# Kernel tuning notes

Measured on AMD Instinct MI355X. Metric: run time of the kernel, lower is better.

Reference implementation:

```python
import jax, jax.numpy as jnp
import numpy as np

N_NODES = 50000
N_EDGES = 1600000
NODE_DIM = 64
HIDDEN_DIM = 128
EDGE_DIM = 32


def _linear_params(key, fan_in, fan_out, bias=True):
    k1, k2 = jax.random.split(key)
    bound = 1.0 / np.sqrt(fan_in)
    W = jax.random.uniform(k1, (fan_in, fan_out), minval=-bound, maxval=bound, dtype=jnp.float32)
    if bias:
        b = jax.random.uniform(k2, (fan_out,), minval=-bound, maxval=bound, dtype=jnp.float32)
        return W, b
    return W, None


def setup_inputs() -> dict:
    key = jax.random.key(0)
    ks = jax.random.split(key, 12)
    h = jax.random.normal(ks[0], (N_NODES, NODE_DIM), dtype=jnp.float32)
    x = jax.random.normal(ks[1], (N_NODES, 3), dtype=jnp.float32) * 10.0
    edge_index = jax.random.randint(ks[2], (2, N_EDGES), 0, N_NODES, dtype=jnp.int32).astype(jnp.int64)
    edge_dist = jax.random.uniform(ks[3], (N_EDGES,), dtype=jnp.float32) * 10.0

    msg_in = 2 * NODE_DIM + EDGE_DIM
    node_w1, node_b1 = _linear_params(ks[4], msg_in, HIDDEN_DIM)
    node_w2, node_b2 = _linear_params(ks[5], HIDDEN_DIM, NODE_DIM)
    coord_w1, coord_b1 = _linear_params(ks[6], msg_in, HIDDEN_DIM)
    coord_w2, _ = _linear_params(ks[7], HIDDEN_DIM, 1, bias=False)
    edge_w1, edge_b1 = _linear_params(ks[8], 1, EDGE_DIM)
    edge_w2, edge_b2 = _linear_params(ks[9], EDGE_DIM, EDGE_DIM)

    return dict(h=h, x=x, edge_index=edge_index, edge_dist=edge_dist,
                node_w1=node_w1, node_b1=node_b1, node_w2=node_w2, node_b2=node_b2,
                coord_w1=coord_w1, coord_b1=coord_b1, coord_w2=coord_w2,
                edge_w1=edge_w1, edge_b1=edge_b1, edge_w2=edge_w2, edge_b2=edge_b2)


def reference(h, x, edge_index, edge_dist,
              node_w1, node_b1, node_w2, node_b2,
              coord_w1, coord_b1, coord_w2,
              edge_w1, edge_b1, edge_w2, edge_b2):
    src = edge_index[0]
    dst = edge_index[1]

    # edge_mlp: Linear(1, edge_dim) -> SiLU -> Linear(edge_dim, edge_dim)
    edge_attr = jax.nn.silu(edge_dist[:, None] @ edge_w1 + edge_b1) @ edge_w2 + edge_b2

    # per-edge message input: [E, 2*node_dim + edge_dim]
    m_input = jnp.concatenate([h[src], h[dst], edge_attr], axis=-1)

    # node_mlp: Linear -> SiLU -> Linear
    m = jax.nn.silu(m_input @ node_w1 + node_b1) @ node_w2 + node_b2
    h_agg = jnp.zeros_like(h).at[dst].add(m)

    # coord_mlp: Linear -> SiLU -> Linear(hidden, 1, bias=False)
    coord_weight = jax.nn.silu(m_input @ coord_w1 + coord_b1) @ coord_w2  # [E, 1]

    dir_vec = x[src] - x[dst]                               # [E, 3]
    dir_len = jnp.maximum(jnp.linalg.norm(dir_vec, axis=-1, keepdims=True), 1e-8)
    coord_update = coord_weight * (dir_vec / dir_len)
    x_agg = jnp.zeros_like(x).at[dst].add(coord_update)

    return (h + h_agg, x + x_agg)
```

## Files before the change

kernel.cpp:

```cpp
#include <hip/hip_runtime.h>
#include <stdint.h>

#define NN 50000
#define NE 1600000
#define BE 128

typedef __attribute__((ext_vector_type(8))) short short8;
typedef __attribute__((ext_vector_type(4))) float f32x4;

__device__ __forceinline__ unsigned short f2bf(float f) {
    unsigned int u = __float_as_uint(f);
    u += 0x7fff + ((u >> 16) & 1);
    return (unsigned short)(u >> 16);
}

__device__ __forceinline__ float silu_f(float v) {
    return v / (1.0f + __expf(-v));
}

__global__ void prep_kernel(const float* __restrict__ nw1,
                            const float* __restrict__ cw1,
                            const float* __restrict__ nw2,
                            unsigned short* __restrict__ ws) {
    int i = blockIdx.x * 256 + threadIdx.x;
    if (i < 20480) {
        int n = i / 160, k = i % 160;
        ws[i] = f2bf(nw1[k * 128 + n]);
    } else if (i < 40960) {
        int j = i - 20480; int n = j / 160, k = j % 160;
        ws[i] = f2bf(cw1[k * 128 + n]);
    } else if (i < 49152) {
        int j = i - 40960; int o = j / 128, k = j % 128;
        ws[i] = f2bf(nw2[k * 64 + o]);
    }
}

__global__ void init_out(const float4* __restrict__ h4,
                         const float4* __restrict__ x4,
                         float4* __restrict__ out4) {
    int i = blockIdx.x * 256 + threadIdx.x;
    if (i < 800000)       out4[i] = h4[i];
    else if (i < 837500)  out4[i] = x4[i - 800000];
}

#define MIS 168

__global__ __launch_bounds__(256, 3)
void egnn_edge_kernel(const float* __restrict__ h,
                      const float* __restrict__ x,
                      const int* __restrict__ eidx,
                      const float* __restrict__ edist,
                      const float* __restrict__ node_b1,
                      const float* __restrict__ node_b2,
                      const float* __restrict__ coord_b1,
                      const float* __restrict__ coord_w2,
                      const float* __restrict__ ew1,
                      const float* __restrict__ eb1,
                      const float* __restrict__ ew2,
                      const float* __restrict__ eb2,
                      const unsigned short* __restrict__ ws,
                      float* __restrict__ out_h,
                      float* __restrict__ out_x) {
    __shared__ unsigned short mi[BE * MIS];

    const int tid  = threadIdx.x;
    const int w    = tid >> 6;
    const int lane = tid & 63;
    const int ln   = lane & 15;
    const int quad = lane >> 4;
    const int e0   = blockIdx.x * BE;

    {
        const float4* h4 = (const float4*)h;
        const int g = tid >> 4, l16 = tid & 15;
        #pragma unroll
        for (int it = 0; it < 16; ++it) {
            int row = it * 16 + g;
            int e = row & 127;
            int node = (row < 128) ? eidx[e0 + e] : eidx[NE + e0 + e];
            int cbase = (row < 128) ? 0 : 64;
            float4 v = h4[node * 16 + l16];
            unsigned short b[4] = {f2bf(v.x), f2bf(v.y), f2bf(v.z), f2bf(v.w)};
            *(uint2*)&mi[e * MIS + cbase + l16 * 4] = *(uint2*)b;
        }
    }
    {
        int e = tid >> 1, half = tid & 1;
        float d = edist[e0 + e];
        float s[16];
        #pragma unroll
        for (int jj = 0; jj < 16; ++jj) s[jj] = eb2[half * 16 + jj];
        #pragma unroll
        for (int k = 0; k < 32; ++k) {
            float tk = silu_f(d * ew1[k] + eb1[k]);
            const float* r2 = ew2 + k * 32 + half * 16;
            #pragma unroll
            for (int jj = 0; jj < 16; ++jj) s[jj] += tk * r2[jj];
        }
        unsigned short sb[16];
        #pragma unroll
        for (int jj = 0; jj < 16; ++jj) sb[jj] = f2bf(s[jj]);
        *(uint4*)&mi[e * MIS + 128 + half * 16]     = *(uint4*)&sb[0];
        *(uint4*)&mi[e * MIS + 128 + half * 16 + 8] = *(uint4*)&sb[8];
    }

    __syncthreads();

    const int arow0 = (w * 32 + ln) * MIS;
    const int arow1 = (w * 32 + 16 + ln) * MIS;
    const int koff  = quad * 8;
    const f32x4 zero = {0.f, 0.f, 0.f, 0.f};

    short8 aA[5], aB[5];
    #pragma unroll
    for (int kc = 0; kc < 5; ++kc) {
        aA[kc] = *(const short8*)&mi[arow0 + kc * 32 + koff];
        aB[kc] = *(const short8*)&mi[arow1 + kc * 32 + koff];
    }

    const int wvoff = ln * 160 + koff;

    f32x4 accC[2][8];
    #pragma unroll
    for (int a = 0; a < 2; ++a)
        #pragma unroll
        for (int b = 0; b < 8; ++b) accC[a][b] = zero;
    {
        const unsigned short* wsrc = ws + 20480;
        #pragma unroll
        for (int half = 0; half < 2; ++half) {
            #pragma unroll
            for (int kc = 0; kc < 5; ++kc) {
                #pragma unroll
                for (int nt = 0; nt < 4; ++nt) {
                    short8 b = *(const short8*)(wsrc + half * 10240 + nt * 2560
                                                + kc * 32 + wvoff);
                    const int nn = half * 4 + nt;
                    accC[0][nn] = __builtin_amdgcn_mfma_f32_16x16x32_bf16(aA[kc], b, accC[0][nn], 0, 0, 0);
                    accC[1][nn] = __builtin_amdgcn_mfma_f32_16x16x32_bf16(aB[kc], b, accC[1][nn], 0, 0, 0);
                }
            }
        }
    }

    {
        float cw[2][4];
        #pragma unroll
        for (int mt = 0; mt < 2; ++mt)
            #pragma unroll
            for (int r = 0; r < 4; ++r) cw[mt][r] = 0.f;
        #pragma unroll
        for (int nt = 0; nt < 8; ++nt) {
            int col = nt * 16 + ln;
            float b1v = coord_b1[col];
            float w2v = coord_w2[col];
            #pragma unroll
            for (int mt = 0; mt < 2; ++mt)
                #pragma unroll
                for (int r = 0; r < 4; ++r)
                    cw[mt][r] += silu_f(accC[mt][nt][r] + b1v) * w2v;
        }
        #pragma unroll
        for (int off = 1; off < 16; off <<= 1) {
            #pragma unroll
            for (int mt = 0; mt < 2; ++mt)
                #pragma unroll
                for (int r = 0; r < 4; ++r)
                    cw[mt][r] += __shfl_xor(cw[mt][r], off, 64);
        }
        if (ln < 8) {
            const int smt = ln >> 2, sr = ln & 3;
            float cwsel = 0.f;
            #pragma unroll
            for (int mt = 0; mt < 2; ++mt)
                #pragma unroll
                for (int r = 0; r < 4; ++r)
                    cwsel = (mt == smt && r == sr) ? cw[mt][r] : cwsel;
            int lrow = w * 32 + smt * 16 + quad * 4 + sr;
            int s = eidx[e0 + lrow], dn = eidx[NE + e0 + lrow];
            float dx = x[s * 3]     - x[dn * 3];
            float dy = x[s * 3 + 1] - x[dn * 3 + 1];
            float dz = x[s * 3 + 2] - x[dn * 3 + 2];
            float len = fmaxf(sqrtf(dx * dx + dy * dy + dz * dz), 1e-8f);
            float k = cwsel / len;
            atomicAdd(out_x + dn * 3,     k * dx);
            atomicAdd(out_x + dn * 3 + 1, k * dy);
            atomicAdd(out_x + dn * 3 + 2, k * dz);
        }
    }

    f32x4 accN[2][8];
    #pragma unroll
    for (int a = 0; a < 2; ++a)
        #pragma unroll
        for (int b = 0; b < 8; ++b) accN[a][b] = zero;
    {
        const unsigned short* wsrc = ws;
        #pragma unroll
        for (int half = 0; half < 2; ++half) {
            #pragma unroll
            for (int kc = 0; kc < 5; ++kc) {
                #pragma unroll
                for (int nt = 0; nt < 4; ++nt) {
                    short8 b = *(const short8*)(wsrc + half * 10240 + nt * 2560
                                                + kc * 32 + wvoff);
                    const int nn = half * 4 + nt;
                    accN[0][nn] = __builtin_amdgcn_mfma_f32_16x16x32_bf16(aA[kc], b, accN[0][nn], 0, 0, 0);
                    accN[1][nn] = __builtin_amdgcn_mfma_f32_16x16x32_bf16(aB[kc], b, accN[1][nn], 0, 0, 0);
                }
            }
        }
    }

    #pragma unroll
    for (int mt = 0; mt < 2; ++mt) {
        const int rowb = (w * 32 + mt * 16 + quad * 4) * MIS;
        #pragma unroll
        for (int nt = 0; nt < 8; ++nt) {
            int col = nt * 16 + ln;
            float b1v = node_b1[col];
            #pragma unroll
            for (int r = 0; r < 4; ++r)
                mi[rowb + r * MIS + col] = f2bf(silu_f(accN[mt][nt][r] + b1v));
        }
    }

    f32x4 acc2[2][4];
    #pragma unroll
    for (int a = 0; a < 2; ++a)
        #pragma unroll
        for (int b = 0; b < 4; ++b) acc2[a][b] = zero;
    const unsigned short* nw2T = ws + 40960;
    #pragma unroll
    for (int kc = 0; kc < 4; ++kc) {
        short8 a0 = *(const short8*)&mi[arow0 + kc * 32 + koff];
        short8 a1 = *(const short8*)&mi[arow1 + kc * 32 + koff];
        #pragma unroll
        for (int nt = 0; nt < 4; ++nt) {
            short8 b = *(const short8*)(nw2T + (nt * 16 + ln) * 128 + kc * 32 + koff);
            acc2[0][nt] = __builtin_amdgcn_mfma_f32_16x16x32_bf16(a0, b, acc2[0][nt], 0, 0, 0);
            acc2[1][nt] = __builtin_amdgcn_mfma_f32_16x16x32_bf16(a1, b, acc2[1][nt], 0, 0, 0);
        }
    }
    #pragma unroll
    for (int mt = 0; mt < 2; ++mt) {
        #pragma unroll
        for (int r = 0; r < 4; ++r) {
            int lrow = w * 32 + mt * 16 + quad * 4 + r;
            int dn = eidx[NE + e0 + lrow];
            float* outrow = out_h + (size_t)dn * 64;
            #pragma unroll
            for (int nt = 0; nt < 4; ++nt) {
                int col = nt * 16 + ln;
                atomicAdd(outrow + col, acc2[mt][nt][r] + node_b2[col]);
            }
        }
    }
}

extern "C" void kernel_launch(void* const* d_in, const int* in_sizes, int n_in,
                              void* d_out, int out_size, void* d_ws, size_t ws_size,
                              hipStream_t stream) {
    const float* h    = (const float*)d_in[0];
    const float* x    = (const float*)d_in[1];
    const int*   eidx = (const int*)d_in[2];
    const float* edist= (const float*)d_in[3];
    const float* nw1  = (const float*)d_in[4];
    const float* nb1  = (const float*)d_in[5];
    const float* nw2  = (const float*)d_in[6];
    const float* nb2  = (const float*)d_in[7];
    const float* cw1  = (const float*)d_in[8];
    const float* cb1  = (const float*)d_in[9];
    const float* cw2  = (const float*)d_in[10];
    const float* ew1  = (const float*)d_in[11];
    const float* eb1  = (const float*)d_in[12];
    const float* ew2  = (const float*)d_in[13];
    const float* eb2  = (const float*)d_in[14];
    float* out = (float*)d_out;
    unsigned short* ws = (unsigned short*)d_ws;

    prep_kernel<<<192, 256, 0, stream>>>(nw1, cw1, nw2, ws);
    init_out<<<3272, 256, 0, stream>>>((const float4*)h, (const float4*)x, (float4*)out);
    egnn_edge_kernel<<<NE / BE, 256, 0, stream>>>(h, x, eidx, edist,
                                                  nb1, nb2, cb1, cw2,
                                                  ew1, eb1, ew2, eb2,
                                                  ws, out, out + 3200000);
}
```

Before: 832.5 us.

## Sort edges by destination and pre-reduce messages in shared memory before atomics

Adds a counting-sort pipeline (histogram, single-block scan, atomic scatter) that builds a permutation grouping edges by destination node. The edge kernel processes edges in that order, stages per-edge messages in shared memory, and sums runs of equal destinations before one atomicAdd per run, cutting global atomic traffic on out_h. It costs four extra launches, a serial 1024-thread scan over 50k nodes, an extra indirection on every edge load, and source-node gathers that are now less coalesced. The scatter order within each destination is nondeterministic.

```diff
diff --git a/kernel.cpp b/kernel.cpp
--- a/kernel.cpp
+++ b/kernel.cpp
@@ -17,6 +17,10 @@
 __device__ __forceinline__ float silu_f(float v) {
     return v / (1.0f + __expf(-v));
 }
+
+#define WS_HIST_B 98304
+#define WS_PERM_B 299008
+#define WS_NEED_B 6699008
 
 __global__ void prep_kernel(const float* __restrict__ nw1,
                             const float* __restrict__ cw1,
@@ -43,6 +47,53 @@
     else if (i < 837500)  out4[i] = x4[i - 800000];
 }
 
+__global__ void zero_hist(int* __restrict__ hist) {
+    int i = blockIdx.x * 256 + threadIdx.x;
+    if (i < NN) hist[i] = 0;
+}
+
+__global__ void hist_kernel(const int* __restrict__ eidx, int* __restrict__ hist) {
+    int e = blockIdx.x * 256 + threadIdx.x;
+    if (e < NE) atomicAdd(&hist[eidx[NE + e]], 1);
+}
+
+__global__ __launch_bounds__(1024)
+void scan_kernel(int* __restrict__ hist) {
+    __shared__ int tmp[1024];
+    __shared__ int carry;
+    const int tid = threadIdx.x;
+    if (tid == 0) carry = 0;
+    __syncthreads();
+    for (int base = 0; base < NN; base += 1024) {
+        int v = (base + tid < NN) ? hist[base + tid] : 0;
+        tmp[tid] = v;
+        __syncthreads();
+        #pragma unroll
+        for (int off = 1; off < 1024; off <<= 1) {
+            int t = (tid >= off) ? tmp[tid - off] : 0;
+            __syncthreads();
+            tmp[tid] += t;
+            __syncthreads();
+        }
+        int excl = carry + tmp[tid] - v;
+        if (base + tid < NN) hist[base + tid] = excl;
+        __syncthreads();
+        if (tid == 1023) carry += tmp[1023];
+        __syncthreads();
+    }
+}
+
+__global__ void scatter_kernel(const int* __restrict__ eidx,
+                               int* __restrict__ offs,
+                               int* __restrict__ perm) {
+    int e = blockIdx.x * 256 + threadIdx.x;
+    if (e < NE) {
+        int d = eidx[NE + e];
+        int p = atomicAdd(&offs[d], 1);
+        perm[p] = e;
+    }
+}
+
 #define MIS 168
 
 __global__ __launch_bounds__(256, 3)
@@ -59,9 +110,14 @@
                       const float* __restrict__ ew2,
                       const float* __restrict__ eb2,
                       const unsigned short* __restrict__ ws,
+                      const int* __restrict__ perm,
                       float* __restrict__ out_h,
                       float* __restrict__ out_x) {
     __shared__ unsigned short mi[BE * MIS];
+    __shared__ int peS[BE];
+    __shared__ int dstS[BE];
+    __shared__ int headsS[BE];
+    __shared__ int nheads;
 
     const int tid  = threadIdx.x;
     const int w    = tid >> 6;
@@ -70,6 +126,11 @@
     const int quad = lane >> 4;
     const int e0   = blockIdx.x * BE;
 
+    if (tid < BE) peS[tid] = perm ? perm[e0 + tid] : (e0 + tid);
+    if (tid == 0) nheads = 0;
+    __syncthreads();
+    if (tid < BE) dstS[tid] = eidx[NE + peS[tid]];
+
     {
         const float4* h4 = (const float4*)h;
         const int g = tid >> 4, l16 = tid & 15;
@@ -77,7 +138,8 @@
         for (int it = 0; it < 16; ++it) {
             int row = it * 16 + g;
             int e = row & 127;
-            int node = (row < 128) ? eidx[e0 + e] : eidx[NE + e0 + e];
+            int pe = peS[e];
+            int node = (row < 128) ? eidx[pe] : eidx[NE + pe];
             int cbase = (row < 128) ? 0 : 64;
             float4 v = h4[node * 16 + l16];
             unsigned short b[4] = {f2bf(v.x), f2bf(v.y), f2bf(v.z), f2bf(v.w)};
@@ -86,7 +148,7 @@
     }
     {
         int e = tid >> 1, half = tid & 1;
-        float d = edist[e0 + e];
+        float d = edist[peS[e]];
         float s[16];
         #pragma unroll
         for (int jj = 0; jj < 16; ++jj) s[jj] = eb2[half * 16 + jj];
@@ -177,7 +239,7 @@
                 for (int r = 0; r < 4; ++r)
                     cwsel = (mt == smt && r == sr) ? cw[mt][r] : cwsel;
             int lrow = w * 32 + smt * 16 + quad * 4 + sr;
-            int s = eidx[e0 + lrow], dn = eidx[NE + e0 + lrow];
+            int s = eidx[peS[lrow]], dn = dstS[lrow];
             float dx = x[s * 3]     - x[dn * 3];
             float dy = x[s * 3 + 1] - x[dn * 3 + 1];
             float dz = x[s * 3 + 2] - x[dn * 3 + 2];
@@ -242,18 +304,37 @@
             acc2[1][nt] = __builtin_amdgcn_mfma_f32_16x16x32_bf16(a1, b, acc2[1][nt], 0, 0, 0);
         }
     }
+
+    __syncthreads();
+    float* macc = (float*)mi;
     #pragma unroll
     for (int mt = 0; mt < 2; ++mt) {
         #pragma unroll
         for (int r = 0; r < 4; ++r) {
             int lrow = w * 32 + mt * 16 + quad * 4 + r;
-            int dn = eidx[NE + e0 + lrow];
-            float* outrow = out_h + (size_t)dn * 64;
             #pragma unroll
             for (int nt = 0; nt < 4; ++nt) {
                 int col = nt * 16 + ln;
-                atomicAdd(outrow + col, acc2[mt][nt][r] + node_b2[col]);
+                macc[lrow * 64 + col] = acc2[mt][nt][r] + node_b2[col];
             }
+        }
+    }
+    __syncthreads();
+    if (tid < BE) {
+        bool isHead = (tid == 0) || (dstS[tid] != dstS[tid - 1]);
+        if (isHead) { int k = atomicAdd(&nheads, 1); headsS[k] = tid; }
+    }
+    __syncthreads();
+    {
+        const int nh = nheads;
+        for (int k = w; k < nh; k += 4) {
+            int i = headsS[k];
+            int d = dstS[i];
+            int jend = i + 1;
+            while (jend < BE && dstS[jend] == d) ++jend;
+            float sum = 0.f;
+            for (int r = i; r < jend; ++r) sum += macc[r * 64 + lane];
+            atomicAdd(out_h + (size_t)d * 64 + lane, sum);
         }
     }
 }
@@ -281,8 +362,20 @@
 
     prep_kernel<<<192, 256, 0, stream>>>(nw1, cw1, nw2, ws);
     init_out<<<3272, 256, 0, stream>>>((const float4*)h, (const float4*)x, (float4*)out);
+
+    const int* perm = nullptr;
+    if (ws_size >= (size_t)WS_NEED_B) {
+        int* hist  = (int*)((char*)d_ws + WS_HIST_B);
+        int* permw = (int*)((char*)d_ws + WS_PERM_B);
+        zero_hist<<<196, 256, 0, stream>>>(hist);
+        hist_kernel<<<NE / 256, 256, 0, stream>>>(eidx, hist);
+        scan_kernel<<<1, 1024, 0, stream>>>(hist);
+        scatter_kernel<<<NE / 256, 256, 0, stream>>>(eidx, hist, permw);
+        perm = permw;
+    }
+
     egnn_edge_kernel<<<NE / BE, 256, 0, stream>>>(h, x, eidx, edist,
                                                   nb1, nb2, cb1, cw2,
                                                   ew1, eb1, ew2, eb2,
-                                                  ws, out, out + 3200000);
-}
+                                                  ws, perm, out, out + 3200000);
+}
```

New measurement: 1.460 ms. 75.4% more time.
